# Performance work log

Hardware: AMD Instinct MI355X
Metric: run time of the kernel (lower is better)

## Reference

```python
import jax, jax.numpy as jnp
import numpy as np

B, S, D = 2, 2048, 1024   # batch, seq, hidden_dim
I = 512                   # intermediate_dim (per-expert FFN width)
E = 16                    # num_experts
TOP_K = 2


def setup_inputs() -> dict:
    key = jax.random.key(0)
    ks = jax.random.split(key, 10)
    sc_d = 1.0 / np.sqrt(D)
    sc_i = 1.0 / np.sqrt(I)
    return {
        "x": jax.random.normal(ks[0], (B, S, D), dtype=jnp.float32),
        # router gate: Linear(D -> E) with bias (nnx.Linear default)
        "gate_w": jax.random.normal(ks[1], (D, E), dtype=jnp.float32) * sc_d,
        "gate_b": jnp.zeros((E,), dtype=jnp.float32),
        # shared expert MLP (SwiGLU: down(silu(gate(x)) * up(x)))
        "shared_wg": jax.random.normal(ks[2], (D, I), dtype=jnp.float32) * sc_d,
        "shared_wu": jax.random.normal(ks[3], (D, I), dtype=jnp.float32) * sc_d,
        "shared_wd": jax.random.normal(ks[4], (I, D), dtype=jnp.float32) * sc_i,
        # routed experts, stacked on leading E axis
        "experts_wg": jax.random.normal(ks[5], (E, D, I), dtype=jnp.float32) * sc_d,
        "experts_wu": jax.random.normal(ks[6], (E, D, I), dtype=jnp.float32) * sc_d,
        "experts_wd": jax.random.normal(ks[7], (E, I, D), dtype=jnp.float32) * sc_i,
    }


def _mlp(x, wg, wu, wd):
    # SwiGLU MLP: down(silu(gate(x)) * up(x))
    return jnp.einsum("bsi,id->bsd", jax.nn.silu(x @ wg) * (x @ wu), wd)


def reference(x, gate_w, gate_b, shared_wg, shared_wu, shared_wd,
              experts_wg, experts_wu, experts_wd):
    # router: sigmoid logits -> top_k -> normalize by sum of selected scores
    router_logits = jax.nn.sigmoid(x @ gate_w + gate_b)          # [B,S,E]
    expert_values, expert_indices = jax.lax.top_k(router_logits, k=TOP_K)
    expert_values = expert_values / jnp.sum(expert_values, axis=-1, keepdims=True)

    # dense all-expert compute (faithful to source): [B,S,E,D]
    hg = jnp.einsum("bsd,edi->bsei", x, experts_wg)
    hu = jnp.einsum("bsd,edi->bsei", x, experts_wu)
    all_outputs = jnp.einsum("bsei,eid->bsed", jax.nn.silu(hg) * hu, experts_wd)

    # gather top-k expert outputs: [B,S,K,D]
    selected = jnp.take_along_axis(all_outputs, expert_indices[..., None], axis=2)
    expert_weighted = jnp.sum(expert_values[..., None] * selected, axis=2)  # [B,S,D]

    return x + _mlp(x, shared_wg, shared_wu, shared_wd) + expert_weighted
```

## Files before the change

### kernel.cpp

```cpp
#include <hip/hip_runtime.h>
#include <stdint.h>

typedef __attribute__((ext_vector_type(8))) short short8;
typedef __attribute__((ext_vector_type(4))) float f32x4;

#define TOKENS 4096
#define DDIM 1024
#define IDIM 512
#define NEXP 16
#define NEXP1 17
#define NSLOTS 12288
#define CSTRIDE 32

#define OFF_WGU   0ull
#define OFF_WD    35651584ull
#define OFF_XB    53477376ull
#define OFF_HGU   61865984ull
#define OFF_H     87031808ull
#define OFF_TOK   99614720ull
#define OFF_WT    99893248ull
#define OFF_CNT   100171776ull
#define OFF_BASE  100175872ull

__device__ __forceinline__ float bf2f(unsigned short u) {
    union { uint32_t i; float f; } v; v.i = ((uint32_t)u) << 16; return v.f;
}
__device__ __forceinline__ unsigned short f2bf(float f) {
    union { float f; uint32_t i; } v; v.f = f;
    uint32_t r = v.i + 0x7FFFu + ((v.i >> 16) & 1u);
    return (unsigned short)(r >> 16);
}

__global__ void k_transpose(const float* __restrict__ eg, const float* __restrict__ eu,
                            const float* __restrict__ ed, const float* __restrict__ sg,
                            const float* __restrict__ su, const float* __restrict__ sd,
                            unsigned short* __restrict__ Wgu, unsigned short* __restrict__ Wd)
{
    int z = blockIdx.z;
    int e = z / 3, m = z % 3;
    int R = (m == 2) ? 512 : 1024;
    int C = (m == 2) ? 1024 : 512;
    int r0 = blockIdx.y * 32, c0 = blockIdx.x * 32;
    if (r0 >= R || c0 >= C) return;
    const float* src;
    if (m == 0)      src = (e < 16) ? eg + (size_t)e * 524288 : sg;
    else if (m == 1) src = (e < 16) ? eu + (size_t)e * 524288 : su;
    else             src = (e < 16) ? ed + (size_t)e * 524288 : sd;

    __shared__ float tl[32][33];
    int c = threadIdx.x & 31, r = threadIdx.x >> 5;
    #pragma unroll
    for (int rr = 0; rr < 4; ++rr)
        tl[r + rr * 8][c] = src[(size_t)(r0 + r + rr * 8) * C + (c0 + c)];
    __syncthreads();
    #pragma unroll
    for (int rr = 0; rr < 4; ++rr) {
        int n = c0 + r + rr * 8;
        int k = r0 + c;
        unsigned short hv = f2bf(tl[c][r + rr * 8]);
        if (m < 2) Wgu[(size_t)e * 1048576 + (size_t)(n + (m == 1 ? 512 : 0)) * 1024 + k] = hv;
        else       Wd [(size_t)e * 524288  + (size_t)n * 512 + k] = hv;
    }
}

__global__ void k_xconv(const float* __restrict__ x, unsigned short* __restrict__ xb,
                        float* __restrict__ out, int* __restrict__ tok, float* __restrict__ wt)
{
    int i = blockIdx.x * 256 + threadIdx.x;
    float4 v = ((const float4*)x)[i];
    ((float4*)out)[i] = v;
    ushort4 b;
    b.x = f2bf(v.x); b.y = f2bf(v.y); b.z = f2bf(v.z); b.w = f2bf(v.w);
    ((ushort4*)xb)[i] = b;
    if (i < TOKENS) { tok[16 * 4096 + i] = i; wt[16 * 4096 + i] = 1.0f; }
}

__global__ __launch_bounds__(512, 4)
void k_router(const float* __restrict__ x, const float* __restrict__ gw,
              const float* __restrict__ gb, int* __restrict__ tok,
              float* __restrict__ wt, int* __restrict__ counts)
{
    __shared__ float gws[1024 * 12];

    const int t = blockIdx.x * 8 + (threadIdx.x >> 6);
    const int lane = threadIdx.x & 63;
    const float* xr = x + (size_t)t * DDIM;

    float xv[16];
    #pragma unroll
    for (int kk = 0; kk < 16; ++kk) xv[kk] = xr[kk * 64 + lane];

    float v[16];

    for (int p = 0; p < 2; ++p) {
        __syncthreads();
        #pragma unroll
        for (int c = 0; c < 4; ++c) {
            int idx = threadIdx.x + c * 512;
            int k = idx >> 1;
            int h = (idx & 1) * 4;
            float4 g4 = *(const float4*)(gw + k * 16 + p * 8 + h);
            *(float4*)&gws[k * 12 + h] = g4;
        }
        __syncthreads();

        double a[8];
        #pragma unroll
        for (int j = 0; j < 8; ++j) a[j] = 0.0;

        #pragma unroll
        for (int kk = 0; kk < 16; ++kk) {
            int kl = kk * 64 + lane;
            float4 gA = *(const float4*)&gws[kl * 12];
            float4 gB = *(const float4*)&gws[kl * 12 + 4];
            double xd = (double)xv[kk];
            a[0] += xd * (double)gA.x; a[1] += xd * (double)gA.y;
            a[2] += xd * (double)gA.z; a[3] += xd * (double)gA.w;
            a[4] += xd * (double)gB.x; a[5] += xd * (double)gB.y;
            a[6] += xd * (double)gB.z; a[7] += xd * (double)gB.w;
        }

        #pragma unroll
        for (int off = 32; off > 0; off >>= 1) {
            #pragma unroll
            for (int j = 0; j < 8; ++j)
                a[j] += __shfl_xor(a[j], off, 64);
        }

        #pragma unroll
        for (int j = 0; j < 8; ++j)
            v[p * 8 + j] = 1.0f / (1.0f + expf(-(float)(a[j] + (double)gb[p * 8 + j])));
    }

    if (lane == 0) {
        int i0 = 0;
        #pragma unroll
        for (int e = 1; e < 16; ++e) if (v[e] > v[i0]) i0 = e;
        int i1 = (i0 == 0) ? 1 : 0;
        #pragma unroll
        for (int e = 0; e < 16; ++e) if (e != i0 && e != i1 && v[e] > v[i1]) i1 = e;
        float s = v[i0] + v[i1];
        float w0 = v[i0] / s, w1 = v[i1] / s;
        int p0 = atomicAdd(&counts[i0 * CSTRIDE], 1);
        tok[i0 * 4096 + p0] = t; wt[i0 * 4096 + p0] = w0;
        int p1 = atomicAdd(&counts[i1 * CSTRIDE], 1);
        tok[i1 * 4096 + p1] = t; wt[i1 * 4096 + p1] = w1;
    }
}

__global__ void k_prefix(int* counts, int* bases)
{
    if (threadIdx.x == 0 && blockIdx.x == 0) {
        counts[16 * CSTRIDE] = TOKENS;
        int a = 0;
        for (int e = 0; e < NEXP1; ++e) { bases[e] = a; a += counts[e * CSTRIDE]; }
        bases[17] = a;
    }
}

template <int MODE>
__global__ __launch_bounds__(256, 2)
void k_gemm(const unsigned short* __restrict__ Amat, const unsigned short* __restrict__ Bmat,
            const int* __restrict__ tok, const float* __restrict__ wt,
            const int* __restrict__ counts, const int* __restrict__ bases,
            unsigned short* __restrict__ Hgu, float* __restrict__ out)
{
    constexpr int K = (MODE == 0) ? 1024 : 512;
    const int e = blockIdx.z;
    const int cnt = counts[e * CSTRIDE];
    const int m0 = blockIdx.y * 128;
    if (m0 >= cnt) return;
    const int n0 = blockIdx.x * 128;
    const int base = bases[e];

    __shared__ unsigned short As[128 * 40];
    __shared__ unsigned short Bs[128 * 40];

    const int tid = threadIdx.x;
    const int seg = tid & 3;
    const int hrow = tid >> 2;

    const unsigned short* aptr[2];
    const unsigned short* bptr[2];
    unsigned short* asd[2];
    unsigned short* bsd[2];
    #pragma unroll
    for (int it = 0; it < 2; ++it) {
        int row = hrow + it * 64;
        int rc = m0 + row; if (rc > cnt - 1) rc = cnt - 1;
        size_t rowidx;
        if (MODE == 0) rowidx = (size_t)tok[e * 4096 + rc];
        else           rowidx = (size_t)(base + rc);
        aptr[it] = Amat + rowidx * K + seg * 8;
        bptr[it] = Bmat + (size_t)e * 1024 * K + (size_t)(n0 + row) * K + seg * 8;
        asd[it] = &As[row * 40 + seg * 8];
        bsd[it] = &Bs[row * 40 + seg * 8];
    }

    const int wave = tid >> 6;
    const int lane = tid & 63;
    const int wm = wave & 1, wn = wave >> 1;
    const int q = lane >> 4, mc = lane & 15;

    f32x4 acc[4][4];
    #pragma unroll
    for (int i = 0; i < 4; ++i)
        #pragma unroll
        for (int j = 0; j < 4; ++j) acc[i][j] = (f32x4){0.f, 0.f, 0.f, 0.f};

    for (int k0 = 0; k0 < K; k0 += 32) {
        uint4 av0 = *(const uint4*)(aptr[0] + k0);
        uint4 av1 = *(const uint4*)(aptr[1] + k0);
        uint4 bv0 = *(const uint4*)(bptr[0] + k0);
        uint4 bv1 = *(const uint4*)(bptr[1] + k0);
        __syncthreads();
        *(uint4*)asd[0] = av0;
        *(uint4*)asd[1] = av1;
        *(uint4*)bsd[0] = bv0;
        *(uint4*)bsd[1] = bv1;
        __syncthreads();
        short8 a[4], b[4];
        #pragma unroll
        for (int i = 0; i < 4; ++i)
            a[i] = *(const short8*)&As[(wm * 64 + i * 16 + mc) * 40 + q * 8];
        #pragma unroll
        for (int j = 0; j < 4; ++j)
            b[j] = *(const short8*)&Bs[(wn * 64 + j * 16 + mc) * 40 + q * 8];
        #pragma unroll
        for (int i = 0; i < 4; ++i)
            #pragma unroll
            for (int j = 0; j < 4; ++j)
                acc[i][j] = __builtin_amdgcn_mfma_f32_16x16x32_bf16(a[i], b[j], acc[i][j], 0, 0, 0);
    }

    #pragma unroll
    for (int i = 0; i < 4; ++i) {
        int lrow = wm * 64 + i * 16 + q * 4;
        #pragma unroll
        for (int r = 0; r < 4; ++r) {
            int mrow = m0 + lrow + r;
            if (mrow >= cnt) continue;
            if (MODE == 0) {
                size_t rowoff = (size_t)(base + mrow) * 1024;
                #pragma unroll
                for (int j = 0; j < 4; ++j) {
                    int gc = n0 + wn * 64 + j * 16 + mc;
                    Hgu[rowoff + gc] = f2bf(acc[i][j][r]);
                }
            } else {
                int t = tok[e * 4096 + mrow];
                float w = wt[e * 4096 + mrow];
                size_t rowoff = (size_t)t * 1024;
                #pragma unroll
                for (int j = 0; j < 4; ++j) {
                    int gc = n0 + wn * 64 + j * 16 + mc;
                    atomicAdd(&out[rowoff + gc], w * acc[i][j][r]);
                }
            }
        }
    }
}

__global__ void k_silu(const unsigned short* __restrict__ Hgu, unsigned short* __restrict__ H)
{
    int gid = blockIdx.x * 256 + threadIdx.x;
    int s = gid >> 6;
    int c = (gid & 63) * 8;
    const unsigned short* g = Hgu + (size_t)s * 1024 + c;
    unsigned short gg[8], uu[8], oo[8];
    *(uint4*)gg = *(const uint4*)g;
    *(uint4*)uu = *(const uint4*)(g + 512);
    #pragma unroll
    for (int j = 0; j < 8; ++j) {
        float gv = bf2f(gg[j]);
        float uv = bf2f(uu[j]);
        float sv = gv / (1.0f + __expf(-gv));
        oo[j] = f2bf(sv * uv);
    }
    *(uint4*)(H + (size_t)s * 512 + c) = *(uint4*)oo;
}

extern "C" void kernel_launch(void* const* d_in, const int* in_sizes, int n_in,
                              void* d_out, int out_size, void* d_ws, size_t ws_size,
                              hipStream_t stream)
{
    const float* x  = (const float*)d_in[0];
    const float* gw = (const float*)d_in[1];
    const float* gb = (const float*)d_in[2];
    const float* sg = (const float*)d_in[3];
    const float* su = (const float*)d_in[4];
    const float* sd = (const float*)d_in[5];
    const float* eg = (const float*)d_in[6];
    const float* eu = (const float*)d_in[7];
    const float* ed = (const float*)d_in[8];
    float* out = (float*)d_out;
    char* ws = (char*)d_ws;

    unsigned short* Wgu = (unsigned short*)(ws + OFF_WGU);
    unsigned short* Wd  = (unsigned short*)(ws + OFF_WD);
    unsigned short* xb  = (unsigned short*)(ws + OFF_XB);
    unsigned short* Hgu = (unsigned short*)(ws + OFF_HGU);
    unsigned short* H   = (unsigned short*)(ws + OFF_H);
    int*   tok   = (int*)(ws + OFF_TOK);
    float* wt    = (float*)(ws + OFF_WT);
    int*   counts= (int*)(ws + OFF_CNT);
    int*   bases = (int*)(ws + OFF_BASE);

    hipMemsetAsync(counts, 0, 4096, stream);
    k_transpose<<<dim3(32, 32, 51), 256, 0, stream>>>(eg, eu, ed, sg, su, sd, Wgu, Wd);
    k_xconv<<<4096, 256, 0, stream>>>(x, xb, out, tok, wt);
    k_router<<<512, 512, 0, stream>>>(x, gw, gb, tok, wt, counts);
    k_prefix<<<1, 64, 0, stream>>>(counts, bases);
    k_gemm<0><<<dim3(8, 32, 17), 256, 0, stream>>>(xb, Wgu, tok, wt, counts, bases, Hgu, out);
    k_silu<<<3072, 256, 0, stream>>>(Hgu, H);
    k_gemm<1><<<dim3(8, 32, 17), 256, 0, stream>>>(H, Wd, tok, wt, counts, bases, Hgu, out);
}
```

Baseline: 319.3 us.

## Replace atomic scatter with combine kernel and use direct global-to-LDS loads

The down-projection GEMM now writes bf16 per-slot results into a buffer instead of doing float atomicAdd into the output. A new combine kernel gathers the two routed slots and the shared slot per token, adds x, and writes the output once, so xconv no longer copies x into out. The GEMM tile loads switch to global_load_lds (direct global-to-LDS 16-byte copies) with an unpadded 32-wide LDS layout, and occupancy is raised to 3 blocks per SM. The intent is to remove atomic contention and register staging, at the cost of an extra kernel, bf16 rounding of expert outputs before combining, and possible LDS bank conflicts from the removed padding.

```diff
diff --git a/kernel.cpp b/kernel.cpp
--- a/kernel.cpp
+++ b/kernel.cpp
@@ -9,7 +9,6 @@
 #define IDIM 512
 #define NEXP 16
 #define NEXP1 17
-#define NSLOTS 12288
 #define CSTRIDE 32
 
 #define OFF_WGU   0ull
@@ -18,7 +17,8 @@
 #define OFF_HGU   61865984ull
 #define OFF_H     87031808ull
 #define OFF_TOK   99614720ull
-#define OFF_WT    99893248ull
+#define OFF_REC   99893248ull
+#define OFF_WREC  99926016ull
 #define OFF_CNT   100171776ull
 #define OFF_BASE  100175872ull
 
@@ -29,6 +29,11 @@
     union { float f; uint32_t i; } v; v.f = f;
     uint32_t r = v.i + 0x7FFFu + ((v.i >> 16) & 1u);
     return (unsigned short)(r >> 16);
+}
+__device__ __forceinline__ void cp16(const unsigned short* g, unsigned short* l) {
+    __builtin_amdgcn_global_load_lds(
+        (const __attribute__((address_space(1))) uint32_t*)g,
+        (__attribute__((address_space(3))) uint32_t*)l, 16, 0, 0);
 }
 
 __global__ void k_transpose(const float* __restrict__ eg, const float* __restrict__ eu,
@@ -64,21 +69,21 @@
 }
 
 __global__ void k_xconv(const float* __restrict__ x, unsigned short* __restrict__ xb,
-                        float* __restrict__ out, int* __restrict__ tok, float* __restrict__ wt)
+                        int* __restrict__ tok)
 {
     int i = blockIdx.x * 256 + threadIdx.x;
     float4 v = ((const float4*)x)[i];
-    ((float4*)out)[i] = v;
     ushort4 b;
     b.x = f2bf(v.x); b.y = f2bf(v.y); b.z = f2bf(v.z); b.w = f2bf(v.w);
     ((ushort4*)xb)[i] = b;
-    if (i < TOKENS) { tok[16 * 4096 + i] = i; wt[16 * 4096 + i] = 1.0f; }
+    if (i < TOKENS) tok[16 * 4096 + i] = i;
 }
 
 __global__ __launch_bounds__(512, 4)
 void k_router(const float* __restrict__ x, const float* __restrict__ gw,
               const float* __restrict__ gb, int* __restrict__ tok,
-              float* __restrict__ wt, int* __restrict__ counts)
+              int2* __restrict__ rec, float2* __restrict__ wrec,
+              int* __restrict__ counts)
 {
     __shared__ float gws[1024 * 12];
 
@@ -142,9 +147,11 @@
         float s = v[i0] + v[i1];
         float w0 = v[i0] / s, w1 = v[i1] / s;
         int p0 = atomicAdd(&counts[i0 * CSTRIDE], 1);
-        tok[i0 * 4096 + p0] = t; wt[i0 * 4096 + p0] = w0;
+        tok[i0 * 4096 + p0] = t;
         int p1 = atomicAdd(&counts[i1 * CSTRIDE], 1);
-        tok[i1 * 4096 + p1] = t; wt[i1 * 4096 + p1] = w1;
+        tok[i1 * 4096 + p1] = t;
+        rec[t]  = make_int2(i0 * 4096 + p0, i1 * 4096 + p1);
+        wrec[t] = make_float2(w0, w1);
     }
 }
 
@@ -159,11 +166,10 @@
 }
 
 template <int MODE>
-__global__ __launch_bounds__(256, 2)
+__global__ __launch_bounds__(256, 3)
 void k_gemm(const unsigned short* __restrict__ Amat, const unsigned short* __restrict__ Bmat,
-            const int* __restrict__ tok, const float* __restrict__ wt,
-            const int* __restrict__ counts, const int* __restrict__ bases,
-            unsigned short* __restrict__ Hgu, float* __restrict__ out)
+            const int* __restrict__ tok, const int* __restrict__ counts,
+            const int* __restrict__ bases, unsigned short* __restrict__ Hgu)
 {
     constexpr int K = (MODE == 0) ? 1024 : 512;
     const int e = blockIdx.z;
@@ -173,32 +179,31 @@
     const int n0 = blockIdx.x * 128;
     const int base = bases[e];
 
-    __shared__ unsigned short As[128 * 40];
-    __shared__ unsigned short Bs[128 * 40];
-
-    const int tid = threadIdx.x;
-    const int seg = tid & 3;
-    const int hrow = tid >> 2;
-
-    const unsigned short* aptr[2];
-    const unsigned short* bptr[2];
-    unsigned short* asd[2];
-    unsigned short* bsd[2];
-    #pragma unroll
-    for (int it = 0; it < 2; ++it) {
-        int row = hrow + it * 64;
-        int rc = m0 + row; if (rc > cnt - 1) rc = cnt - 1;
-        size_t rowidx;
-        if (MODE == 0) rowidx = (size_t)tok[e * 4096 + rc];
-        else           rowidx = (size_t)(base + rc);
-        aptr[it] = Amat + rowidx * K + seg * 8;
-        bptr[it] = Bmat + (size_t)e * 1024 * K + (size_t)(n0 + row) * K + seg * 8;
-        asd[it] = &As[row * 40 + seg * 8];
-        bsd[it] = &Bs[row * 40 + seg * 8];
-    }
-
+    __shared__ unsigned short As[128 * 32];
+    __shared__ unsigned short Bs[128 * 32];
+
+    const int tid  = threadIdx.x;
     const int wave = tid >> 6;
     const int lane = tid & 63;
+    const int lrow = lane >> 2;
+    const int lseg = lane & 3;
+
+    unsigned short* a_dst0 = &As[wave * 1024];
+    unsigned short* a_dst1 = &As[wave * 1024 + 512];
+    unsigned short* b_dst0 = &Bs[wave * 1024];
+    unsigned short* b_dst1 = &Bs[wave * 1024 + 512];
+
+    int ar0 = m0 + wave * 32 + lrow;      if (ar0 > cnt - 1) ar0 = cnt - 1;
+    int ar1 = m0 + wave * 32 + 16 + lrow; if (ar1 > cnt - 1) ar1 = cnt - 1;
+    size_t ai0, ai1;
+    if (MODE == 0) { ai0 = (size_t)tok[e * 4096 + ar0]; ai1 = (size_t)tok[e * 4096 + ar1]; }
+    else           { ai0 = (size_t)(base + ar0);        ai1 = (size_t)(base + ar1); }
+    const unsigned short* ag0 = Amat + ai0 * K + lseg * 8;
+    const unsigned short* ag1 = Amat + ai1 * K + lseg * 8;
+    const size_t eoff = (size_t)e * 1024 * K;
+    const unsigned short* bg0 = Bmat + eoff + (size_t)(n0 + wave * 32 + lrow) * K + lseg * 8;
+    const unsigned short* bg1 = Bmat + eoff + (size_t)(n0 + wave * 32 + 16 + lrow) * K + lseg * 8;
+
     const int wm = wave & 1, wn = wave >> 1;
     const int q = lane >> 4, mc = lane & 15;
 
@@ -209,23 +214,19 @@
         for (int j = 0; j < 4; ++j) acc[i][j] = (f32x4){0.f, 0.f, 0.f, 0.f};
 
     for (int k0 = 0; k0 < K; k0 += 32) {
-        uint4 av0 = *(const uint4*)(aptr[0] + k0);
-        uint4 av1 = *(const uint4*)(aptr[1] + k0);
-        uint4 bv0 = *(const uint4*)(bptr[0] + k0);
-        uint4 bv1 = *(const uint4*)(bptr[1] + k0);
         __syncthreads();
-        *(uint4*)asd[0] = av0;
-        *(uint4*)asd[1] = av1;
-        *(uint4*)bsd[0] = bv0;
-        *(uint4*)bsd[1] = bv1;
+        cp16(ag0 + k0, a_dst0);
+        cp16(ag1 + k0, a_dst1);
+        cp16(bg0 + k0, b_dst0);
+        cp16(bg1 + k0, b_dst1);
         __syncthreads();
         short8 a[4], b[4];
         #pragma unroll
         for (int i = 0; i < 4; ++i)
-            a[i] = *(const short8*)&As[(wm * 64 + i * 16 + mc) * 40 + q * 8];
+            a[i] = *(const short8*)&As[(wm * 64 + i * 16 + mc) * 32 + q * 8];
         #pragma unroll
         for (int j = 0; j < 4; ++j)
-            b[j] = *(const short8*)&Bs[(wn * 64 + j * 16 + mc) * 40 + q * 8];
+            b[j] = *(const short8*)&Bs[(wn * 64 + j * 16 + mc) * 32 + q * 8];
         #pragma unroll
         for (int i = 0; i < 4; ++i)
             #pragma unroll
@@ -235,27 +236,16 @@
 
     #pragma unroll
     for (int i = 0; i < 4; ++i) {
-        int lrow = wm * 64 + i * 16 + q * 4;
+        int lr = wm * 64 + i * 16 + q * 4;
         #pragma unroll
         for (int r = 0; r < 4; ++r) {
-            int mrow = m0 + lrow + r;
+            int mrow = m0 + lr + r;
             if (mrow >= cnt) continue;
-            if (MODE == 0) {
-                size_t rowoff = (size_t)(base + mrow) * 1024;
-                #pragma unroll
-                for (int j = 0; j < 4; ++j) {
-                    int gc = n0 + wn * 64 + j * 16 + mc;
-                    Hgu[rowoff + gc] = f2bf(acc[i][j][r]);
-                }
-            } else {
-                int t = tok[e * 4096 + mrow];
-                float w = wt[e * 4096 + mrow];
-                size_t rowoff = (size_t)t * 1024;
-                #pragma unroll
-                for (int j = 0; j < 4; ++j) {
-                    int gc = n0 + wn * 64 + j * 16 + mc;
-                    atomicAdd(&out[rowoff + gc], w * acc[i][j][r]);
-                }
+            size_t rowoff = (size_t)(base + mrow) * 1024;
+            #pragma unroll
+            for (int j = 0; j < 4; ++j) {
+                int gc = n0 + wn * 64 + j * 16 + mc;
+                Hgu[rowoff + gc] = f2bf(acc[i][j][r]);
             }
         }
     }
@@ -278,6 +268,32 @@
         oo[j] = f2bf(sv * uv);
     }
     *(uint4*)(H + (size_t)s * 512 + c) = *(uint4*)oo;
+}
+
+__global__ void k_combine(const float* __restrict__ x, const unsigned short* __restrict__ Hs,
+                          const int2* __restrict__ rec, const float2* __restrict__ wrec,
+                          const int* __restrict__ bases, float* __restrict__ out)
+{
+    int t = blockIdx.x * 2 + (threadIdx.x >> 7);
+    int c = (threadIdx.x & 127) * 8;
+    int2 r = rec[t];
+    float2 w = wrec[t];
+    int s0 = bases[r.x >> 12] + (r.x & 4095);
+    int s1 = bases[r.y >> 12] + (r.y & 4095);
+    int ss = 8192 + t;
+
+    unsigned short h0[8], h1[8], hs[8];
+    *(uint4*)h0 = *(const uint4*)(Hs + (size_t)s0 * 1024 + c);
+    *(uint4*)h1 = *(const uint4*)(Hs + (size_t)s1 * 1024 + c);
+    *(uint4*)hs = *(const uint4*)(Hs + (size_t)ss * 1024 + c);
+    const float* xr = x + (size_t)t * 1024 + c;
+    float o[8];
+    #pragma unroll
+    for (int j = 0; j < 8; ++j)
+        o[j] = xr[j] + bf2f(hs[j]) + w.x * bf2f(h0[j]) + w.y * bf2f(h1[j]);
+    float* orow = out + (size_t)t * 1024 + c;
+    *(float4*)orow       = *(float4*)&o[0];
+    *(float4*)(orow + 4) = *(float4*)&o[4];
 }
 
 extern "C" void kernel_launch(void* const* d_in, const int* in_sizes, int n_in,
@@ -301,17 +317,19 @@
     unsigned short* xb  = (unsigned short*)(ws + OFF_XB);
     unsigned short* Hgu = (unsigned short*)(ws + OFF_HGU);
     unsigned short* H   = (unsigned short*)(ws + OFF_H);
-    int*   tok   = (int*)(ws + OFF_TOK);
-    float* wt    = (float*)(ws + OFF_WT);
-    int*   counts= (int*)(ws + OFF_CNT);
-    int*   bases = (int*)(ws + OFF_BASE);
+    int*    tok   = (int*)(ws + OFF_TOK);
+    int2*   rec   = (int2*)(ws + OFF_REC);
+    float2* wrec  = (float2*)(ws + OFF_WREC);
+    int*    counts= (int*)(ws + OFF_CNT);
+    int*    bases = (int*)(ws + OFF_BASE);
 
     hipMemsetAsync(counts, 0, 4096, stream);
     k_transpose<<<dim3(32, 32, 51), 256, 0, stream>>>(eg, eu, ed, sg, su, sd, Wgu, Wd);
-    k_xconv<<<4096, 256, 0, stream>>>(x, xb, out, tok, wt);
-    k_router<<<512, 512, 0, stream>>>(x, gw, gb, tok, wt, counts);
+    k_xconv<<<4096, 256, 0, stream>>>(x, xb, tok);
+    k_router<<<512, 512, 0, stream>>>(x, gw, gb, tok, rec, wrec, counts);
     k_prefix<<<1, 64, 0, stream>>>(counts, bases);
-    k_gemm<0><<<dim3(8, 32, 17), 256, 0, stream>>>(xb, Wgu, tok, wt, counts, bases, Hgu, out);
+    k_gemm<0><<<dim3(8, 32, 17), 256, 0, stream>>>(xb, Wgu, tok, counts, bases, Hgu);
     k_silu<<<3072, 256, 0, stream>>>(Hgu, H);
-    k_gemm<1><<<dim3(8, 32, 17), 256, 0, stream>>>(H, Wd, tok, wt, counts, bases, Hgu, out);
-}
+    k_gemm<1><<<dim3(8, 32, 17), 256, 0, stream>>>(H, Wd, tok, counts, bases, Hgu);
+    k_combine<<<2048, 256, 0, stream>>>(x, Hgu, rec, wrec, bases, out);
+}
```

Measured after the change: 293.2 us. -8.2%, faster.
